# Optimization experiments

Hardware: AMD Instinct MI355X
Metric: run time of the kernel (lower is better)

The kernel has to match this reference:

```python
import jax, jax.numpy as jnp
import numpy as np

EPS = 1e-12
LAMDA = 1.0
MAX_ITER = 10


def setup_inputs() -> dict:
    key = jax.random.key(0)
    k1, k2 = jax.random.split(key)
    B, L1, L2, D = 64, 1024, 1024, 256
    x1 = jax.random.normal(k1, (B, L1, D), dtype=jnp.float32)
    x2 = jax.random.normal(k2, (B, L2, D), dtype=jnp.float32)
    return {"x1": x1, "x2": x2}


def _cos(x1, x2):
    # batched cosine similarity: [B, L1, L2]
    M = jnp.einsum('bik,bjk->bij', x1, x2)
    a = jnp.sqrt(jnp.sum(x1 * x1, axis=-1, keepdims=True))  # [B, L1, 1]
    b = jnp.sqrt(jnp.sum(x2 * x2, axis=-1, keepdims=True))  # [B, L2, 1]
    norm = a * jnp.swapaxes(b, 1, 2)                          # [B, L1, L2]
    return M / (norm + EPS)


def reference(x1, x2):
    B, L1, _ = x1.shape
    L2 = x2.shape[1]
    M = 1.0 - _cos(x1, x2)          # [B, L1, L2] cost matrix
    K = jnp.exp(-M * LAMDA)
    w1 = jnp.full((B, L1, 1), 1.0 / L1, dtype=x1.dtype)
    w2 = jnp.full((B, L2, 1), 1.0 / L2, dtype=x1.dtype)
    ui = jnp.ones((B, L1, 1), dtype=x1.dtype)
    vi = jnp.ones((B, L2, 1), dtype=x1.dtype)
    Kt = jnp.swapaxes(K, 1, 2)      # [B, L2, L1]

    def body(_, carry):
        ui, vi = carry
        vi = w2 / (jnp.matmul(Kt, ui) + EPS)
        ui = w1 / (jnp.matmul(K, vi) + EPS)
        return (ui, vi)

    ui, vi = jax.lax.fori_loop(0, MAX_ITER, body, (ui, vi))
    G = ui * K * jnp.swapaxes(vi, 1, 2)   # transport plan [B, L1, L2]
    G_max = jnp.max(G, axis=(-1, -2), keepdims=True)
    G_min = jnp.min(G, axis=(-1, -2), keepdims=True)
    G = (G - G_min) / (G_max - G_min + EPS)
    return G * M
```

## Files before the change

### kernel.cpp

```cpp
#include <hip/hip_runtime.h>
#include <hip/hip_bf16.h>
#include <hip/hip_fp8.h>


#define EPSV 1e-12f
#define W1 0.0009765625f

typedef short  short8 __attribute__((ext_vector_type(8)));
typedef float  f32x4  __attribute__((ext_vector_type(4)));
typedef float  f32x2v __attribute__((ext_vector_type(2)));

__device__ __forceinline__ float rcpf_(float x) {
#if __has_builtin(__builtin_amdgcn_rcpf)
  return __builtin_amdgcn_rcpf(x);
#else
  return 1.0f / x;
#endif
}
__device__ __forceinline__ float rsqf_(float x) {
#if __has_builtin(__builtin_amdgcn_rsqf)
  return __builtin_amdgcn_rsqf(x);
#else
  return rsqrtf(x);
#endif
}

__device__ __forceinline__ unsigned char enc1(float x) {
#if __has_builtin(__builtin_amdgcn_cvt_pk_fp8_f32)
  int v = __builtin_amdgcn_cvt_pk_fp8_f32(x, x, 0, false);
  return (unsigned char)(v & 0xff);
#else
  __hip_fp8_e4m3 q(x); return (unsigned char)q.__x;
#endif
}
__device__ __forceinline__ float dec1(unsigned char b) {
#if __has_builtin(__builtin_amdgcn_cvt_f32_fp8)
  return __builtin_amdgcn_cvt_f32_fp8((int)b, 0);
#else
  __hip_fp8_e4m3 q; q.__x = (__hip_fp8_storage_t)b; return (float)q;
#endif
}
__device__ __forceinline__ unsigned pack4fp8(float a, float b, float c, float d) {
#if __has_builtin(__builtin_amdgcn_cvt_pk_fp8_f32)
  int v = __builtin_amdgcn_cvt_pk_fp8_f32(a, b, 0, false);
  v = __builtin_amdgcn_cvt_pk_fp8_f32(c, d, v, true);
  return (unsigned)v;
#else
  return (unsigned)enc1(a) | ((unsigned)enc1(b) << 8) |
         ((unsigned)enc1(c) << 16) | ((unsigned)enc1(d) << 24);
#endif
}
__device__ __forceinline__ void unpack4fp8(unsigned v, float* f) {
#if __has_builtin(__builtin_amdgcn_cvt_pk_f32_fp8)
  f32x2v p;
  p = __builtin_amdgcn_cvt_pk_f32_fp8((int)v, false); f[0] = p[0]; f[1] = p[1];
  p = __builtin_amdgcn_cvt_pk_f32_fp8((int)v, true);  f[2] = p[0]; f[3] = p[1];
#else
  #pragma unroll
  for (int i = 0; i < 4; ++i) f[i] = dec1((unsigned char)((v >> (i * 8)) & 0xff));
#endif
}
__device__ __forceinline__ void decode16(uint4 d, float* f) {
  unpack4fp8(d.x, f); unpack4fp8(d.y, f + 4);
  unpack4fp8(d.z, f + 8); unpack4fp8(d.w, f + 12);
}
__device__ __forceinline__ float dot16u(uint4 d, const float* s) {
#if __has_builtin(__builtin_amdgcn_cvt_pk_f32_fp8)
  f32x2v p; float a = 0.f;
  p = __builtin_amdgcn_cvt_pk_f32_fp8((int)d.x, false); a += p[0]*s[0]  + p[1]*s[1];
  p = __builtin_amdgcn_cvt_pk_f32_fp8((int)d.x, true);  a += p[0]*s[2]  + p[1]*s[3];
  p = __builtin_amdgcn_cvt_pk_f32_fp8((int)d.y, false); a += p[0]*s[4]  + p[1]*s[5];
  p = __builtin_amdgcn_cvt_pk_f32_fp8((int)d.y, true);  a += p[0]*s[6]  + p[1]*s[7];
  p = __builtin_amdgcn_cvt_pk_f32_fp8((int)d.z, false); a += p[0]*s[8]  + p[1]*s[9];
  p = __builtin_amdgcn_cvt_pk_f32_fp8((int)d.z, true);  a += p[0]*s[10] + p[1]*s[11];
  p = __builtin_amdgcn_cvt_pk_f32_fp8((int)d.w, false); a += p[0]*s[12] + p[1]*s[13];
  p = __builtin_amdgcn_cvt_pk_f32_fp8((int)d.w, true);  a += p[0]*s[14] + p[1]*s[15];
  return a;
#else
  float f[16]; decode16(d, f);
  float a = 0.f;
  #pragma unroll
  for (int k = 0; k < 16; ++k) a += f[k] * s[k];
  return a;
#endif
}
__device__ __forceinline__ void axpy16u(uint4 d, float u, float* pacc) {
#if __has_builtin(__builtin_amdgcn_cvt_pk_f32_fp8)
  f32x2v p;
  p = __builtin_amdgcn_cvt_pk_f32_fp8((int)d.x, false); pacc[0]  += p[0]*u; pacc[1]  += p[1]*u;
  p = __builtin_amdgcn_cvt_pk_f32_fp8((int)d.x, true);  pacc[2]  += p[0]*u; pacc[3]  += p[1]*u;
  p = __builtin_amdgcn_cvt_pk_f32_fp8((int)d.y, false); pacc[4]  += p[0]*u; pacc[5]  += p[1]*u;
  p = __builtin_amdgcn_cvt_pk_f32_fp8((int)d.y, true);  pacc[6]  += p[0]*u; pacc[7]  += p[1]*u;
  p = __builtin_amdgcn_cvt_pk_f32_fp8((int)d.z, false); pacc[8]  += p[0]*u; pacc[9]  += p[1]*u;
  p = __builtin_amdgcn_cvt_pk_f32_fp8((int)d.z, true);  pacc[10] += p[0]*u; pacc[11] += p[1]*u;
  p = __builtin_amdgcn_cvt_pk_f32_fp8((int)d.w, false); pacc[12] += p[0]*u; pacc[13] += p[1]*u;
  p = __builtin_amdgcn_cvt_pk_f32_fp8((int)d.w, true);  pacc[14] += p[0]*u; pacc[15] += p[1]*u;
#else
  float f[16]; decode16(d, f);
  #pragma unroll
  for (int k = 0; k < 16; ++k) pacc[k] += f[k] * u;
#endif
}

__device__ __forceinline__ short8 ld_cvt8_sq(const float* p, float* sq) {
  float4 f0 = *(const float4*)p;
  float4 f1 = *(const float4*)(p + 4);
  *sq += f0.x * f0.x + f0.y * f0.y + f0.z * f0.z + f0.w * f0.w
       + f1.x * f1.x + f1.y * f1.y + f1.z * f1.z + f1.w * f1.w;
  float2 p0; p0.x = f0.x; p0.y = f0.y;
  float2 p1; p1.x = f0.z; p1.y = f0.w;
  float2 p2; p2.x = f1.x; p2.y = f1.y;
  float2 p3; p3.x = f1.z; p3.y = f1.w;
  __hip_bfloat162 h0 = __float22bfloat162_rn(p0);
  __hip_bfloat162 h1 = __float22bfloat162_rn(p1);
  __hip_bfloat162 h2_ = __float22bfloat162_rn(p2);
  __hip_bfloat162 h3 = __float22bfloat162_rn(p3);
  short2 a = *(short2*)&h0, b = *(short2*)&h1, c = *(short2*)&h2_, d = *(short2*)&h3;
  short8 r;
  r[0] = a.x; r[1] = a.y; r[2] = b.x; r[3] = b.y;
  r[4] = c.x; r[5] = c.y; r[6] = d.x; r[7] = d.y;
  return r;
}

__global__ __launch_bounds__(256) void diag_kernel(float* __restrict__ out,
                                                   float val, int n) {
  int stride = gridDim.x * 256;
  for (int i = blockIdx.x * 256 + threadIdx.x; i < n; i += stride) out[i] = val;
}

__global__ __launch_bounds__(256) void gemm_kernel(
    const float* __restrict__ x1, const float* __restrict__ x2,
    unsigned char* __restrict__ K8g, unsigned char* __restrict__ R8g,
    unsigned* __restrict__ mm, _Float16* __restrict__ p0) {
  __shared__ __align__(16) unsigned short smem[2 * 128 * 64];
  __shared__ float asq[128], bsq[128];
  __shared__ float csum[4][128];
  unsigned short* As = smem;
  unsigned short* Bs = smem + 128 * 64;
  int bid = blockIdx.x;
  int b = bid >> 6, tile = bid & 63;
  int ti = (tile >> 3) << 7, tj = (tile & 7) << 7;
  int t = threadIdx.x, lane = t & 63, wave = t >> 6;
  int wr = (wave >> 1) << 6, wc = (wave & 1) << 6;
  const float* Ag = x1 + ((size_t)(b * 1024 + ti)) * 256;
  const float* Bg = x2 + ((size_t)(b * 1024 + tj)) * 256;

  if (bid == 0 && t < 128) mm[t] = (t < 64) ? 0u : 0x7f800000u;

  f32x4 acc[4][4];
  f32x4 zero = {0.f, 0.f, 0.f, 0.f};
  #pragma unroll
  for (int m = 0; m < 4; ++m)
    #pragma unroll
    for (int n = 0; n < 4; ++n) acc[m][n] = zero;

  float sqa[4] = {0.f, 0.f, 0.f, 0.f};
  float sqb[4] = {0.f, 0.f, 0.f, 0.f};
  short8 ra[4], rb[4];
  #pragma unroll
  for (int c = 0; c < 4; ++c) {
    int ch = t + (c << 8); int row = ch >> 3, kg = ch & 7;
    ra[c] = ld_cvt8_sq(Ag + row * 256 + kg * 8, &sqa[c]);
    rb[c] = ld_cvt8_sq(Bg + row * 256 + kg * 8, &sqb[c]);
  }

  for (int k0 = 0; k0 < 4; ++k0) {
    __syncthreads();
    #pragma unroll
    for (int c = 0; c < 4; ++c) {
      int ch = t + (c << 8); int row = ch >> 3, kg = ch & 7;
      int kgs = kg ^ (row & 7);
      *(short8*)(As + row * 64 + kgs * 8) = ra[c];
      *(short8*)(Bs + row * 64 + kgs * 8) = rb[c];
    }
    __syncthreads();
    if (k0 < 3) {
      #pragma unroll
      for (int c = 0; c < 4; ++c) {
        int ch = t + (c << 8); int row = ch >> 3, kg = ch & 7;
        ra[c] = ld_cvt8_sq(Ag + row * 256 + (k0 + 1) * 64 + kg * 8, &sqa[c]);
        rb[c] = ld_cvt8_sq(Bg + row * 256 + (k0 + 1) * 64 + kg * 8, &sqb[c]);
      }
    }
    #pragma unroll
    for (int ks = 0; ks < 2; ++ks) {
      short8 af[4], bfr[4];
      #pragma unroll
      for (int m = 0; m < 4; ++m) {
        int row = wr + m * 16 + (lane & 15);
        int c16 = (ks << 2) + (lane >> 4);
        af[m] = *(const short8*)(As + row * 64 + ((c16 ^ (row & 7)) << 3));
      }
      #pragma unroll
      for (int n = 0; n < 4; ++n) {
        int row = wc + n * 16 + (lane & 15);
        int c16 = (ks << 2) + (lane >> 4);
        bfr[n] = *(const short8*)(Bs + row * 64 + ((c16 ^ (row & 7)) << 3));
      }
      #pragma unroll
      for (int m = 0; m < 4; ++m)
        #pragma unroll
        for (int n = 0; n < 4; ++n)
          acc[m][n] = __builtin_amdgcn_mfma_f32_16x16x32_bf16(bfr[n], af[m], acc[m][n], 0, 0, 0);
    }
  }
  __syncthreads();
  #pragma unroll
  for (int c = 0; c < 4; ++c) {
    float sa = sqa[c], sb = sqb[c];
    sa += __shfl_xor(sa, 1, 64); sb += __shfl_xor(sb, 1, 64);
    sa += __shfl_xor(sa, 2, 64); sb += __shfl_xor(sb, 2, 64);
    sa += __shfl_xor(sa, 4, 64); sb += __shfl_xor(sb, 4, 64);
    if ((t & 7) == 0) {
      int row = (t + (c << 8)) >> 3;
      asq[row] = sa; bsq[row] = sb;
    }
  }
  __syncthreads();

  float ira[4];
  #pragma unroll
  for (int m = 0; m < 4; ++m)
    ira[m] = rsqf_(asq[wr + m * 16 + (lane & 15)]);
  float irb[4][4];
  #pragma unroll
  for (int n = 0; n < 4; ++n)
    #pragma unroll
    for (int q = 0; q < 4; ++q)
      irb[n][q] = rsqf_(bsq[wc + n * 16 + ((lane >> 4) << 2) + q]);
  float csn[4][4];
  #pragma unroll
  for (int n = 0; n < 4; ++n)
    #pragma unroll
    for (int q = 0; q < 4; ++q) csn[n][q] = 0.f;
  size_t kbase = ((size_t)b << 20);
  #pragma unroll
  for (int m = 0; m < 4; ++m) {
    size_t rowoff = kbase + (size_t)(ti + wr + m * 16 + (lane & 15)) * 1024 + tj + wc + ((lane >> 4) << 2);
    #pragma unroll
    for (int n = 0; n < 4; ++n) {
      float kv[4];
      #pragma unroll
      for (int q = 0; q < 4; ++q) {
        float cosv = acc[m][n][q] * ira[m] * irb[n][q];
        kv[q] = __expf(cosv - 1.0f);
        csn[n][q] += kv[q];
      }
      unsigned pk = pack4fp8(kv[0], kv[1], kv[2], kv[3]);
      float kd[4];
      unpack4fp8(pk, kd);
      float rr[4];
      #pragma unroll
      for (int q = 0; q < 4; ++q) rr[q] = kv[q] * rcpf_(kd[q]) - 1.0f;
      unsigned pr = pack4fp8(rr[0], rr[1], rr[2], rr[3]);
      *(unsigned*)(K8g + rowoff + n * 16) = pk;
      *(unsigned*)(R8g + rowoff + n * 16) = pr;
    }
  }
  #pragma unroll
  for (int n = 0; n < 4; ++n)
    #pragma unroll
    for (int q = 0; q < 4; ++q) {
      float c_ = csn[n][q];
      c_ += __shfl_xor(c_, 1, 64);
      c_ += __shfl_xor(c_, 2, 64);
      c_ += __shfl_xor(c_, 4, 64);
      c_ += __shfl_xor(c_, 8, 64);
      if ((lane & 15) == 0)
        csum[wave][wc + n * 16 + ((lane >> 4) << 2) + q] = c_;
    }
  __syncthreads();
  if (t < 128) {
    float s_ = csum[t >> 6][t] + csum[2 + (t >> 6)][t];
    p0[((size_t)b << 13) + ((size_t)(ti >> 7) << 10) + tj + t] = (_Float16)s_;
  }
}

template<int BSHIFT, int NSRC>
__global__ __launch_bounds__(1024) void fused1024_kernel(
    const unsigned char* __restrict__ K8, const _Float16* __restrict__ src,
    _Float16* __restrict__ dst) {
  int bid = blockIdx.x;
  int b = bid >> 2, s = bid & 3;
  int t = threadIdx.x, lane = t & 63, w = t >> 6;
  __shared__ float sv[1024];
  __shared__ float plds[8][1024];
  {
    int col = t;
    const _Float16* sp = src + ((size_t)b << BSHIFT) + col;
    float y = 0.f;
    #pragma unroll
    for (int j = 0; j < NSRC; ++j) y += (float)sp[j << 10];
    sv[col] = W1 / (y + EPSV);
  }
  __syncthreads();
  float svr[16];
  {
    float4 s0 = *(const float4*)&sv[lane * 16];
    float4 s1 = *(const float4*)&sv[lane * 16 + 4];
    float4 s2 = *(const float4*)&sv[lane * 16 + 8];
    float4 s3 = *(const float4*)&sv[lane * 16 + 12];
    svr[0] = s0.x;  svr[1] = s0.y;  svr[2]  = s0.z;  svr[3]  = s0.w;
    svr[4] = s1.x;  svr[5] = s1.y;  svr[6]  = s1.z;  svr[7]  = s1.w;
    svr[8] = s2.x;  svr[9] = s2.y;  svr[10] = s2.z;  svr[11] = s2.w;
    svr[12] = s3.x; svr[13] = s3.y; svr[14] = s3.z;  svr[15] = s3.w;
  }
  float pacc[16];
  #pragma unroll
  for (int k = 0; k < 16; ++k) pacc[k] = 0.f;
  const unsigned char* kp = K8 + ((size_t)b << 20) + (size_t)(s * 256 + w) * 1024 + lane * 16;
  uint4 c0 = *(const uint4*)(kp);
  uint4 c1 = *(const uint4*)(kp + 16384);
  for (int p = 0; p < 8; ++p) {
    uint4 n0, n1_;
    if (p < 7) {
      n0 = *(const uint4*)(kp + (size_t)(2 * p + 2) * 16384);
      n1_ = *(const uint4*)(kp + (size_t)(2 * p + 3) * 16384);
    }
    float d0 = dot16u(c0, svr);
    float d1 = dot16u(c1, svr);
    #pragma unroll
    for (int off = 1; off < 64; off <<= 1) {
      d0 += __shfl_xor(d0, off, 64);
      d1 += __shfl_xor(d1, off, 64);
    }
    float u0 = W1 / (d0 + EPSV);
    float u1 = W1 / (d1 + EPSV);
    axpy16u(c0, u0, pacc);
    axpy16u(c1, u1, pacc);
    c0 = n0; c1 = n1_;
  }
  if (w < 8) {
    *(float4*)&plds[w][lane * 16]      = *(float4*)&pacc[0];
    *(float4*)&plds[w][lane * 16 + 4]  = *(float4*)&pacc[4];
    *(float4*)&plds[w][lane * 16 + 8]  = *(float4*)&pacc[8];
    *(float4*)&plds[w][lane * 16 + 12] = *(float4*)&pacc[12];
  }
  __syncthreads();
  if (w >= 8) {
    float* pl = &plds[w - 8][lane * 16];
    #pragma unroll
    for (int k = 0; k < 16; ++k) pl[k] += pacc[k];
  }
  __syncthreads();
  {
    int col = t;
    float sum = 0.f;
    #pragma unroll
    for (int i = 0; i < 8; ++i) sum += plds[i][col];
    dst[((size_t)b << 12) + (s << 10) + col] = (_Float16)sum;
  }
}

__global__ __launch_bounds__(1024) void fused1024F_kernel(
    const unsigned char* __restrict__ K8, const unsigned char* __restrict__ R8,
    const _Float16* __restrict__ src, float* __restrict__ zb,
    unsigned* __restrict__ mm) {
  int bid = blockIdx.x;
  int b = bid >> 2, s = bid & 3;
  int t = threadIdx.x, lane = t & 63, w = t >> 6;
  __shared__ float sv[1024];
  __shared__ float red[32];
  {
    int col = t;
    const _Float16* sp = src + ((size_t)b << 12) + col;
    float y = (float)sp[0] + (float)sp[1024] + (float)sp[2048] + (float)sp[3072];
    sv[col] = W1 / (y + EPSV);
  }
  __syncthreads();
  float svr[16];
  {
    float4 s0 = *(const float4*)&sv[lane * 16];
    float4 s1 = *(const float4*)&sv[lane * 16 + 4];
    float4 s2 = *(const float4*)&sv[lane * 16 + 8];
    float4 s3 = *(const float4*)&sv[lane * 16 + 12];
    svr[0] = s0.x;  svr[1] = s0.y;  svr[2]  = s0.z;  svr[3]  = s0.w;
    svr[4] = s1.x;  svr[5] = s1.y;  svr[6]  = s1.z;  svr[7]  = s1.w;
    svr[8] = s2.x;  svr[9] = s2.y;  svr[10] = s2.z;  svr[11] = s2.w;
    svr[12] = s3.x; svr[13] = s3.y; svr[14] = s3.z;  svr[15] = s3.w;
  }
  float gmn = 3.4e38f, gmx = 0.f;
  const unsigned char* kp = K8 + ((size_t)b << 20) + (size_t)(s * 256 + w) * 1024 + lane * 16;
  const unsigned char* rp = R8 + ((size_t)b << 20) + (size_t)(s * 256 + w) * 1024 + lane * 16;
  for (int p = 0; p < 8; ++p) {
    uint4 c0 = *(const uint4*)(kp + (size_t)(2 * p) * 16384);
    uint4 c1 = *(const uint4*)(kp + (size_t)(2 * p + 1) * 16384);
    uint4 r0 = *(const uint4*)(rp + (size_t)(2 * p) * 16384);
    uint4 r1 = *(const uint4*)(rp + (size_t)(2 * p + 1) * 16384);
    float kf0[16], kf1[16], rf[16];
    decode16(c0, kf0);
    decode16(r0, rf);
    #pragma unroll
    for (int k = 0; k < 16; ++k) kf0[k] *= (1.0f + rf[k]);
    decode16(c1, kf1);
    decode16(r1, rf);
    #pragma unroll
    for (int k = 0; k < 16; ++k) kf1[k] *= (1.0f + rf[k]);
    float d0 = 0.f, d1 = 0.f;
    #pragma unroll
    for (int k = 0; k < 16; ++k) {
      d0 += kf0[k] * svr[k];
      d1 += kf1[k] * svr[k];
    }
    #pragma unroll
    for (int off = 1; off < 64; off <<= 1) {
      d0 += __shfl_xor(d0, off, 64);
      d1 += __shfl_xor(d1, off, 64);
    }
    float u0 = W1 / (d0 + EPSV);
    float u1 = W1 / (d1 + EPSV);
    if (lane == 0) {
      zb[(b << 10) + s * 256 + w + (2 * p) * 16] = d0;
      zb[(b << 10) + s * 256 + w + (2 * p + 1) * 16] = d1;
    }
    #pragma unroll
    for (int k = 0; k < 16; ++k) {
      float g0 = u0 * kf0[k] * svr[k];
      float g1 = u1 * kf1[k] * svr[k];
      gmn = fminf(gmn, fminf(g0, g1));
      gmx = fmaxf(gmx, fmaxf(g0, g1));
    }
  }
  #pragma unroll
  for (int off = 1; off < 64; off <<= 1) {
    gmn = fminf(gmn, __shfl_xor(gmn, off, 64));
    gmx = fmaxf(gmx, __shfl_xor(gmx, off, 64));
  }
  if (lane == 0) { red[w] = gmn; red[16 + w] = gmx; }
  __syncthreads();
  if (t == 0) {
    float m0 = red[0], m1 = red[16];
    #pragma unroll
    for (int i = 1; i < 16; ++i) { m0 = fminf(m0, red[i]); m1 = fmaxf(m1, red[16 + i]); }
    atomicMin(&mm[64 + b], __float_as_uint(m0));
    atomicMax(&mm[b],      __float_as_uint(m1));
  }
}

__global__ __launch_bounds__(256) void fin_kernel(
    const unsigned char* __restrict__ K8, const unsigned char* __restrict__ R8,
    const _Float16* __restrict__ src, const float* __restrict__ zb,
    const unsigned* __restrict__ mm, float* __restrict__ out) {
  int bid = blockIdx.x;
  int b = bid >> 4, rg = bid & 15;
  int t = threadIdx.x, lane = t & 63, w = t >> 6;
  __shared__ float sv[1024];
  #pragma unroll
  for (int p = 0; p < 4; ++p) {
    int col = (p << 8) + t;
    const _Float16* sp = src + ((size_t)b << 12) + col;
    float y = (float)sp[0] + (float)sp[1024] + (float)sp[2048] + (float)sp[3072];
    sv[col] = W1 / (y + EPSV);
  }
  __syncthreads();
  float svr[16];
  {
    float4 s0 = *(const float4*)&sv[lane * 16];
    float4 s1 = *(const float4*)&sv[lane * 16 + 4];
    float4 s2 = *(const float4*)&sv[lane * 16 + 8];
    float4 s3 = *(const float4*)&sv[lane * 16 + 12];
    svr[0] = s0.x;  svr[1] = s0.y;  svr[2]  = s0.z;  svr[3]  = s0.w;
    svr[4] = s1.x;  svr[5] = s1.y;  svr[6]  = s1.z;  svr[7]  = s1.w;
    svr[8] = s2.x;  svr[9] = s2.y;  svr[10] = s2.z;  svr[11] = s2.w;
    svr[12] = s3.x; svr[13] = s3.y; svr[14] = s3.z;  svr[15] = s3.w;
  }
  float gmx = __uint_as_float(mm[b]);
  float gmn = __uint_as_float(mm[64 + b]);
  float scale = 1.0f / (gmx - gmn + EPSV);
  const unsigned char* kp = K8 + ((size_t)b << 20) + (size_t)(rg * 64 + w) * 1024 + lane * 16;
  const unsigned char* rp = R8 + ((size_t)b << 20) + (size_t)(rg * 64 + w) * 1024 + lane * 16;
  float* op = out + ((size_t)b << 20) + (size_t)(rg * 64 + w) * 1024 + lane * 16;
  for (int it = 0; it < 16; ++it) {
    int r = rg * 64 + w + it * 4;
    float u = W1 / (zb[b * 1024 + r] + EPSV);
    uint4 dk = *(const uint4*)(kp + (size_t)it * 4096);
    uint4 dr = *(const uint4*)(rp + (size_t)it * 4096);
    float kf[16], rf[16], o[16];
    decode16(dk, kf);
    decode16(dr, rf);
    #pragma unroll
    for (int k = 0; k < 16; ++k) {
      float krec = kf[k] * (1.0f + rf[k]);
      float g = u * krec * svr[k];
      o[k] = (g - gmn) * scale * (-__logf(krec));
    }
    *(float4*)(op + (size_t)it * 4096)      = *(float4*)&o[0];
    *(float4*)(op + (size_t)it * 4096 + 4)  = *(float4*)&o[4];
    *(float4*)(op + (size_t)it * 4096 + 8)  = *(float4*)&o[8];
    *(float4*)(op + (size_t)it * 4096 + 12) = *(float4*)&o[12];
  }
}

extern "C" void kernel_launch(void* const* d_in, const int* in_sizes, int n_in,
                              void* d_out, int out_size, void* d_ws, size_t ws_size,
                              hipStream_t stream) {
  const float* x1 = (const float*)d_in[0];
  const float* x2 = (const float*)d_in[1];
  float* out = (float*)d_out;
  char* ws = (char*)d_ws;

  unsigned char* K8g = (unsigned char*)ws;
  unsigned char* R8g = (unsigned char*)(ws + 67108864ULL);
  float*    zb = (float*)(ws + 134217728ULL);
  _Float16* p0 = (_Float16*)(ws + 134217728ULL);
  _Float16* pA = (_Float16*)(ws + 134742016ULL);
  _Float16* pB = (_Float16*)(ws + 135266304ULL);
  unsigned* mm = (unsigned*)(ws + 135790592ULL);
  const size_t WS_NEED = 135791104ULL;

  if (ws_size < WS_NEED) {
    float val = 100.0f + (float)(ws_size >> 20);
    diag_kernel<<<2048, 256, 0, stream>>>(out, val, out_size);
    return;
  }

  gemm_kernel<<<4096, 256, 0, stream>>>(x1, x2, K8g, R8g, mm, p0);
  fused1024_kernel<13, 8><<<256, 1024, 0, stream>>>(K8g, p0, pB);
  for (int k = 2; k <= 9; ++k) {
    _Float16* src = (k & 1) ? pA : pB;
    _Float16* dst = (k & 1) ? pB : pA;
    fused1024_kernel<12, 4><<<256, 1024, 0, stream>>>(K8g, src, dst);
  }
  fused1024F_kernel<<<256, 1024, 0, stream>>>(K8g, R8g, pB, zb, mm);
  fin_kernel<<<1024, 256, 0, stream>>>(K8g, R8g, pB, zb, mm, out);
}
```

Before: 434.6 us.

## Precompute bf16 inputs and norms in prep kernel; DMA tiles directly to LDS

Adds a prep kernel that converts x1/x2 to bf16 and computes inverse row norms, staging them in the output buffer as scratch. The GEMM kernel then loads bf16 tiles straight into LDS with global_load_lds, which drops the register-staged fp32 load, convert and square-sum work from the GEMM. The trade is an extra pass over the fp32 inputs (read plus bf16 write) and an extra launch. The register prefetch double-buffering is also gone, so loads are no longer overlapped with the MFMA work.

```diff
diff --git a/kernel.cpp b/kernel.cpp
--- a/kernel.cpp
+++ b/kernel.cpp
@@ -22,6 +22,17 @@
   return __builtin_amdgcn_rsqf(x);
 #else
   return rsqrtf(x);
+#endif
+}
+
+__device__ __forceinline__ void dma16(const unsigned short* g,
+                                      unsigned short* l, int lane) {
+#if __has_builtin(__builtin_amdgcn_global_load_lds)
+  __builtin_amdgcn_global_load_lds(
+      (const __attribute__((address_space(1))) unsigned*)g,
+      (__attribute__((address_space(3))) unsigned*)l, 16, 0, 0);
+#else
+  *(float4*)((char*)l + lane * 16) = *(const float4*)g;
 #endif
 }
 
@@ -102,50 +113,56 @@
 #endif
 }
 
-__device__ __forceinline__ short8 ld_cvt8_sq(const float* p, float* sq) {
-  float4 f0 = *(const float4*)p;
-  float4 f1 = *(const float4*)(p + 4);
-  *sq += f0.x * f0.x + f0.y * f0.y + f0.z * f0.z + f0.w * f0.w
-       + f1.x * f1.x + f1.y * f1.y + f1.z * f1.z + f1.w * f1.w;
-  float2 p0; p0.x = f0.x; p0.y = f0.y;
-  float2 p1; p1.x = f0.z; p1.y = f0.w;
-  float2 p2; p2.x = f1.x; p2.y = f1.y;
-  float2 p3; p3.x = f1.z; p3.y = f1.w;
-  __hip_bfloat162 h0 = __float22bfloat162_rn(p0);
-  __hip_bfloat162 h1 = __float22bfloat162_rn(p1);
-  __hip_bfloat162 h2_ = __float22bfloat162_rn(p2);
-  __hip_bfloat162 h3 = __float22bfloat162_rn(p3);
-  short2 a = *(short2*)&h0, b = *(short2*)&h1, c = *(short2*)&h2_, d = *(short2*)&h3;
-  short8 r;
-  r[0] = a.x; r[1] = a.y; r[2] = b.x; r[3] = b.y;
-  r[4] = c.x; r[5] = c.y; r[6] = d.x; r[7] = d.y;
-  return r;
-}
-
 __global__ __launch_bounds__(256) void diag_kernel(float* __restrict__ out,
                                                    float val, int n) {
   int stride = gridDim.x * 256;
   for (int i = blockIdx.x * 256 + threadIdx.x; i < n; i += stride) out[i] = val;
 }
 
+__global__ __launch_bounds__(256) void prep_kernel(
+    const float* __restrict__ x1, const float* __restrict__ x2,
+    unsigned short* __restrict__ x1b, unsigned short* __restrict__ x2b,
+    float* __restrict__ ninv1, float* __restrict__ ninv2,
+    unsigned* __restrict__ mm) {
+  int t = threadIdx.x, bid = blockIdx.x;
+  if (bid == 0 && t < 128) mm[t] = (t < 64) ? 0u : 0x7f800000u;
+  int row = bid * 4 + (t >> 6);
+  int lane = t & 63;
+  const float* xp; unsigned short* op; float* np_;
+  int r = row;
+  if (row < 65536) { xp = x1; op = x1b; np_ = ninv1; }
+  else { r = row - 65536; xp = x2; op = x2b; np_ = ninv2; }
+  float4 v = ((const float4*)(xp + (size_t)r * 256))[lane];
+  float s = v.x * v.x + v.y * v.y + v.z * v.z + v.w * v.w;
+  #pragma unroll
+  for (int off = 1; off < 64; off <<= 1) s += __shfl_xor(s, off, 64);
+  if (lane == 0) np_[r] = rsqf_(s);
+  float2 pa; pa.x = v.x; pa.y = v.y;
+  float2 pb; pb.x = v.z; pb.y = v.w;
+  __hip_bfloat162 h0 = __float22bfloat162_rn(pa);
+  __hip_bfloat162 h1 = __float22bfloat162_rn(pb);
+  short2 a2 = *(short2*)&h0, b2 = *(short2*)&h1;
+  ushort4 o;
+  o.x = (unsigned short)a2.x; o.y = (unsigned short)a2.y;
+  o.z = (unsigned short)b2.x; o.w = (unsigned short)b2.y;
+  ((ushort4*)(op + (size_t)r * 256))[lane] = o;
+}
+
 __global__ __launch_bounds__(256) void gemm_kernel(
-    const float* __restrict__ x1, const float* __restrict__ x2,
+    const unsigned short* __restrict__ x1b, const unsigned short* __restrict__ x2b,
+    const float* __restrict__ ninv1, const float* __restrict__ ninv2,
     unsigned char* __restrict__ K8g, unsigned char* __restrict__ R8g,
-    unsigned* __restrict__ mm, _Float16* __restrict__ p0) {
-  __shared__ __align__(16) unsigned short smem[2 * 128 * 64];
-  __shared__ float asq[128], bsq[128];
+    _Float16* __restrict__ p0) {
+  __shared__ __align__(16) unsigned short As[128 * 64];
+  __shared__ __align__(16) unsigned short Bs[128 * 64];
   __shared__ float csum[4][128];
-  unsigned short* As = smem;
-  unsigned short* Bs = smem + 128 * 64;
   int bid = blockIdx.x;
   int b = bid >> 6, tile = bid & 63;
   int ti = (tile >> 3) << 7, tj = (tile & 7) << 7;
   int t = threadIdx.x, lane = t & 63, wave = t >> 6;
   int wr = (wave >> 1) << 6, wc = (wave & 1) << 6;
-  const float* Ag = x1 + ((size_t)(b * 1024 + ti)) * 256;
-  const float* Bg = x2 + ((size_t)(b * 1024 + tj)) * 256;
-
-  if (bid == 0 && t < 128) mm[t] = (t < 64) ? 0u : 0x7f800000u;
+  const unsigned short* Agb = x1b + (size_t)(b * 1024 + ti) * 256;
+  const unsigned short* Bgb = x2b + (size_t)(b * 1024 + tj) * 256;
 
   f32x4 acc[4][4];
   f32x4 zero = {0.f, 0.f, 0.f, 0.f};
@@ -154,34 +171,19 @@
     #pragma unroll
     for (int n = 0; n < 4; ++n) acc[m][n] = zero;
 
-  float sqa[4] = {0.f, 0.f, 0.f, 0.f};
-  float sqb[4] = {0.f, 0.f, 0.f, 0.f};
-  short8 ra[4], rb[4];
-  #pragma unroll
-  for (int c = 0; c < 4; ++c) {
-    int ch = t + (c << 8); int row = ch >> 3, kg = ch & 7;
-    ra[c] = ld_cvt8_sq(Ag + row * 256 + kg * 8, &sqa[c]);
-    rb[c] = ld_cvt8_sq(Bg + row * 256 + kg * 8, &sqb[c]);
-  }
+  int lr8 = lane >> 3;
+  int pce = lane & 7;
+  int sp = pce ^ lr8;
 
   for (int k0 = 0; k0 < 4; ++k0) {
+    #pragma unroll
+    for (int j = 0; j < 4; ++j) {
+      int row0 = (wave << 5) + (j << 3);
+      int rowA = row0 + lr8;
+      dma16(Agb + (size_t)rowA * 256 + k0 * 64 + sp * 8, As + (row0 << 6), lane);
+      dma16(Bgb + (size_t)rowA * 256 + k0 * 64 + sp * 8, Bs + (row0 << 6), lane);
+    }
     __syncthreads();
-    #pragma unroll
-    for (int c = 0; c < 4; ++c) {
-      int ch = t + (c << 8); int row = ch >> 3, kg = ch & 7;
-      int kgs = kg ^ (row & 7);
-      *(short8*)(As + row * 64 + kgs * 8) = ra[c];
-      *(short8*)(Bs + row * 64 + kgs * 8) = rb[c];
-    }
-    __syncthreads();
-    if (k0 < 3) {
-      #pragma unroll
-      for (int c = 0; c < 4; ++c) {
-        int ch = t + (c << 8); int row = ch >> 3, kg = ch & 7;
-        ra[c] = ld_cvt8_sq(Ag + row * 256 + (k0 + 1) * 64 + kg * 8, &sqa[c]);
-        rb[c] = ld_cvt8_sq(Bg + row * 256 + (k0 + 1) * 64 + kg * 8, &sqb[c]);
-      }
-    }
     #pragma unroll
     for (int ks = 0; ks < 2; ++ks) {
       short8 af[4], bfr[4];
@@ -203,31 +205,19 @@
         for (int n = 0; n < 4; ++n)
           acc[m][n] = __builtin_amdgcn_mfma_f32_16x16x32_bf16(bfr[n], af[m], acc[m][n], 0, 0, 0);
     }
-  }
-  __syncthreads();
-  #pragma unroll
-  for (int c = 0; c < 4; ++c) {
-    float sa = sqa[c], sb = sqb[c];
-    sa += __shfl_xor(sa, 1, 64); sb += __shfl_xor(sb, 1, 64);
-    sa += __shfl_xor(sa, 2, 64); sb += __shfl_xor(sb, 2, 64);
-    sa += __shfl_xor(sa, 4, 64); sb += __shfl_xor(sb, 4, 64);
-    if ((t & 7) == 0) {
-      int row = (t + (c << 8)) >> 3;
-      asq[row] = sa; bsq[row] = sb;
-    }
-  }
-  __syncthreads();
+    __syncthreads();
+  }
 
   float ira[4];
   #pragma unroll
   for (int m = 0; m < 4; ++m)
-    ira[m] = rsqf_(asq[wr + m * 16 + (lane & 15)]);
+    ira[m] = ninv1[(size_t)b * 1024 + ti + wr + m * 16 + (lane & 15)];
   float irb[4][4];
   #pragma unroll
   for (int n = 0; n < 4; ++n)
     #pragma unroll
     for (int q = 0; q < 4; ++q)
-      irb[n][q] = rsqf_(bsq[wc + n * 16 + ((lane >> 4) << 2) + q]);
+      irb[n][q] = ninv2[(size_t)b * 1024 + tj + wc + n * 16 + ((lane >> 4) << 2) + q];
   float csn[4][4];
   #pragma unroll
   for (int n = 0; n < 4; ++n)
@@ -508,13 +498,19 @@
   unsigned* mm = (unsigned*)(ws + 135790592ULL);
   const size_t WS_NEED = 135791104ULL;
 
+  unsigned short* x1b  = (unsigned short*)d_out;
+  unsigned short* x2b  = x1b + 16777216;
+  float*          ninv1 = (float*)((char*)d_out + 67108864ULL);
+  float*          ninv2 = (float*)((char*)d_out + 67371008ULL);
+
   if (ws_size < WS_NEED) {
     float val = 100.0f + (float)(ws_size >> 20);
     diag_kernel<<<2048, 256, 0, stream>>>(out, val, out_size);
     return;
   }
 
-  gemm_kernel<<<4096, 256, 0, stream>>>(x1, x2, K8g, R8g, mm, p0);
+  prep_kernel<<<32768, 256, 0, stream>>>(x1, x2, x1b, x2b, ninv1, ninv2, mm);
+  gemm_kernel<<<4096, 256, 0, stream>>>(x1b, x2b, ninv1, ninv2, K8g, R8g, p0);
   fused1024_kernel<13, 8><<<256, 1024, 0, stream>>>(K8g, p0, pB);
   for (int k = 2; k <= 9; ++k) {
     _Float16* src = (k & 1) ? pA : pB;
```

Result: faster. 401.4 us (-7.7%).
